# Kernel optimization log

Hardware: AMD Instinct MI355X
Metric: run time of the kernel (lower is better)

The kernel has to match this reference:

```python
import jax, jax.numpy as jnp
from jax import lax
import numpy as np

B, T, H, W = 8, 32, 128, 128
D_MODEL, D_STATE, D_CONV, EXPAND = 256, 16, 4, 2
D_INNER = EXPAND * D_MODEL
DT_RANK = 16  # ceil(d_model/16)
CHANS = [3, 32, 64, 96]
COV_SCALE = 0.01


def setup_inputs() -> dict:
    key = jax.random.key(0)
    ks = iter(jax.random.split(key, 64))
    def n(shape, s=0.02):
        return jax.random.normal(next(ks), shape, dtype=jnp.float32) * s
    inp = {
        "frames": jax.random.normal(next(ks), (B, T, 3, H, W), dtype=jnp.float32),
        "target_bboxes": jax.random.uniform(next(ks), (B, T, 4), dtype=jnp.float32),
    }
    for i in range(3):
        inp[f"conv_w{i}"] = n((CHANS[i + 1], CHANS[i], 3, 3, 3))
        inp[f"conv_b{i}"] = jnp.zeros((CHANS[i + 1],), jnp.float32)
        inp[f"bn_g{i}"] = jnp.ones((CHANS[i + 1],), jnp.float32)
        inp[f"bn_b{i}"] = jnp.zeros((CHANS[i + 1],), jnp.float32)
    inp["ep_w"] = n((D_MODEL, CHANS[-1])); inp["ep_b"] = jnp.zeros((D_MODEL,), jnp.float32)
    inp["bp1_w"] = n((64, 4), 0.1); inp["bp1_b"] = jnp.zeros((64,), jnp.float32)
    inp["bp2_w"] = n((D_MODEL, 64)); inp["bp2_b"] = jnp.zeros((D_MODEL,), jnp.float32)
    inp["in_proj_w"] = n((2 * D_INNER, D_MODEL))
    inp["conv1d_w"] = n((D_INNER, 1, D_CONV), 0.1)
    inp["conv1d_b"] = jnp.zeros((D_INNER,), jnp.float32)
    inp["x_proj_w"] = n((DT_RANK + 2 * D_STATE, D_INNER))
    inp["dt_proj_w"] = n((D_INNER, DT_RANK), 0.1)
    inp["dt_proj_b"] = jnp.full((D_INNER,), -3.0, jnp.float32)
    inp["A_log"] = jnp.log(jnp.broadcast_to(jnp.arange(1, D_STATE + 1, dtype=jnp.float32), (D_INNER, D_STATE)))
    inp["D_param"] = jnp.ones((D_INNER,), jnp.float32)
    inp["out_proj_w"] = n((D_MODEL, D_INNER))
    inp["h1_w"] = n((D_MODEL // 2, D_MODEL)); inp["h1_b"] = jnp.zeros((D_MODEL // 2,), jnp.float32)
    inp["h2_w"] = n((4, D_MODEL // 2), 0.1); inp["h2_b"] = jnp.zeros((4,), jnp.float32)
    inp["kf_F"] = jnp.eye(4, dtype=jnp.float32) + n((4, 4), 0.01)
    inp["kf_H"] = jnp.eye(4, dtype=jnp.float32) + n((4, 4), 0.01)
    inp["kf_log_q"] = n((4,), 1.0) - 2.0
    inp["kf_log_r"] = n((4,), 1.0) - 2.0
    return inp


DN3D = ("NCDHW", "OIDHW", "NCDHW")


def _forward(frames, target_bboxes, conv_w0, conv_b0, bn_g0, bn_b0,
             conv_w1, conv_b1, bn_g1, bn_b1, conv_w2, conv_b2, bn_g2, bn_b2,
             ep_w, ep_b, bp1_w, bp1_b, bp2_w, bp2_b,
             in_proj_w, conv1d_w, conv1d_b, x_proj_w, dt_proj_w, dt_proj_b,
             A_log, D_param, out_proj_w, h1_w, h1_b, h2_w, h2_b,
             kf_F, kf_H, kf_log_q, kf_log_r):
    Bn, Tn = frames.shape[0], frames.shape[1]

    # ---- bbox_proj: Linear(4,64) -> ReLU -> Linear(64,d_model) ----
    bf = jax.nn.relu(target_bboxes @ bp1_w.T + bp1_b) @ bp2_w.T + bp2_b  # (B,T,Dm)

    # ---- 3D conv encoder (BN in eval mode: running stats 0/1 -> affine only) ----
    x = jnp.transpose(frames, (0, 2, 1, 3, 4))  # (B,C,T,H,W)
    for (w, b, g, be) in ((conv_w0, conv_b0, bn_g0, bn_b0),
                          (conv_w1, conv_b1, bn_g1, bn_b1),
                          (conv_w2, conv_b2, bn_g2, bn_b2)):
        x = lax.conv_general_dilated(x, w, (1, 2, 2), ((1, 1), (1, 1), (1, 1)),
                                     dimension_numbers=DN3D) + b[None, :, None, None, None]
        x = g[None, :, None, None, None] * x + be[None, :, None, None, None]
        x = jax.nn.relu(x)
        x = lax.reduce_window(x, -jnp.inf, lax.max, (1, 1, 1, 2, 2), (1, 1, 1, 2, 2), "VALID")
    x = x.mean(axis=(3, 4))                    # AdaptiveAvgPool3d((None,1,1)) -> (B,Cenc,T)
    ff = jnp.transpose(x, (0, 2, 1)) @ ep_w.T + ep_b  # (B,T,Dm)

    u = ff + bf

    # ---- Mamba block ----
    xz = u @ in_proj_w.T                        # (B,T,2*Di)
    xm, z = jnp.split(xz, 2, axis=-1)
    xc = jnp.transpose(xm, (0, 2, 1))           # (B,Di,T)
    xc = lax.conv_general_dilated(xc, conv1d_w, (1,), ((D_CONV - 1, 0),),
                                  dimension_numbers=("NCW", "OIW", "NCW"),
                                  feature_group_count=D_INNER) + conv1d_b[None, :, None]
    xs = jax.nn.silu(jnp.transpose(xc, (0, 2, 1)))  # (B,T,Di)
    xdbl = xs @ x_proj_w.T
    dt, Bm, Cm = jnp.split(xdbl, [DT_RANK, DT_RANK + D_STATE], axis=-1)
    dt = jax.nn.softplus(dt @ dt_proj_w.T + dt_proj_b)    # (B,T,Di)
    A = -jnp.exp(A_log)                                    # (Di,Ds)
    dA = jnp.exp(dt[..., None] * A)                        # (B,T,Di,Ds)
    dBx = dt[..., None] * Bm[:, :, None, :] * xs[..., None]

    def ssm_step(h, inputs):
        dA_t, dBx_t, C_t = inputs
        h = dA_t * h + dBx_t                               # (B,Di,Ds)
        y = jnp.einsum("bds,bs->bd", h, C_t)
        return h, y

    h0 = jnp.zeros((Bn, D_INNER, D_STATE), xs.dtype)
    _, ys = lax.scan(ssm_step, h0, (jnp.transpose(dA, (1, 0, 2, 3)),
                                    jnp.transpose(dBx, (1, 0, 2, 3)),
                                    jnp.transpose(Cm, (1, 0, 2))))
    y = jnp.transpose(ys, (1, 0, 2)) + D_param * xs
    y = y * jax.nn.silu(z)
    mo = y @ out_proj_w.T                                  # (B,T,Dm)

    # ---- measurement head ----
    meas = jax.nn.sigmoid(jax.nn.relu(mo @ h1_w.T + h1_b) @ h2_w.T + h2_b)  # (B,T,4)

    # ---- Kalman filter over T (scan) ----
    Q = jnp.diag(jnp.exp(kf_log_q) + 1e-6)
    R = jnp.diag(jnp.exp(kf_log_r) + 1e-6)
    I4 = jnp.eye(4, dtype=meas.dtype)
    Hb = jnp.broadcast_to(kf_H, (Bn, 4, 4))

    def kf_step(carry, m_t):
        s, P = carry
        s_pred = jnp.einsum("ij,bjk->bik", kf_F, s)
        P_pred = jnp.einsum("ij,bjk,lk->bil", kf_F, P, kf_F) + Q
        yres = m_t - jnp.einsum("ij,bjk->bik", kf_H, s_pred)
        S = jnp.einsum("ij,bjk,lk->bil", kf_H, P_pred, kf_H) + R
        SinvH = jnp.linalg.solve(S, Hb)                    # S^{-1} H
        K = jnp.einsum("bij,bkj->bik", P_pred, SinvH)      # P H^T S^{-T}
        s_new = s_pred + K @ yres
        IKH = I4 - K @ kf_H
        P_new = IKH @ P_pred @ jnp.swapaxes(IKH, -1, -2) + (K @ R) @ jnp.swapaxes(K, -1, -2)
        return (s_new, P_new), s_new[..., 0]

    state0 = target_bboxes[:, 0, :, None]                  # (B,4,1)
    cov0 = jnp.broadcast_to(I4 * COV_SCALE, (Bn, 4, 4))
    _, preds = lax.scan(kf_step, (state0, cov0), jnp.transpose(meas, (1, 0, 2))[..., None])
    kf_pred = jnp.transpose(preds, (1, 0, 2))              # (B,T,4)
    return kf_pred, meas


def reference(frames, target_bboxes, conv_w0, conv_b0, bn_g0, bn_b0,
              conv_w1, conv_b1, bn_g1, bn_b1, conv_w2, conv_b2, bn_g2, bn_b2,
              ep_w, ep_b, bp1_w, bp1_b, bp2_w, bp2_b,
              in_proj_w, conv1d_w, conv1d_b, x_proj_w, dt_proj_w, dt_proj_b,
              A_log, D_param, out_proj_w, h1_w, h1_b, h2_w, h2_b,
              kf_F, kf_H, kf_log_q, kf_log_r):
    return _forward(frames, target_bboxes, conv_w0, conv_b0, bn_g0, bn_b0,
                    conv_w1, conv_b1, bn_g1, bn_b1, conv_w2, conv_b2, bn_g2, bn_b2,
                    ep_w, ep_b, bp1_w, bp1_b, bp2_w, bp2_b,
                    in_proj_w, conv1d_w, conv1d_b, x_proj_w, dt_proj_w, dt_proj_b,
                    A_log, D_param, out_proj_w, h1_w, h1_b, h2_w, h2_b,
                    kf_F, kf_H, kf_log_q, kf_log_r)
```

## Files before the change

### kernel.cpp

```cpp
#include <hip/hip_runtime.h>
#include <math.h>

constexpr int Bn = 8, Tn = 32;
constexpr int D_INNER = 512;

typedef __attribute__((ext_vector_type(8))) short short8;
typedef __attribute__((ext_vector_type(8))) unsigned short ushort8;
typedef __attribute__((ext_vector_type(4))) float f32x4;

__device__ inline unsigned short f2bf(float x) {
    unsigned int u = __float_as_uint(x);
    unsigned int r = (u + 0x7FFF + ((u >> 16) & 1)) >> 16;
    return (unsigned short)r;
}

__device__ __forceinline__ float kf_mm(float Av, float Bv, int i, int j, int gb) {
    float c = 0.f;
    #pragma unroll
    for (int k = 0; k < 4; ++k)
        c = fmaf(__shfl(Av, gb + i * 4 + k, 64), __shfl(Bv, gb + k * 4 + j, 64), c);
    return c;
}
__device__ __forceinline__ float kf_mmT(float Av, float Bv, int i, int j, int gb) {
    float c = 0.f;
    #pragma unroll
    for (int k = 0; k < 4; ++k)
        c = fmaf(__shfl(Av, gb + i * 4 + k, 64), __shfl(Bv, gb + j * 4 + k, 64), c);
    return c;
}

__global__ void prep_all(
    const float* __restrict__ cw0, const float* __restrict__ cw1,
    const float* __restrict__ cw2,
    const float* __restrict__ ip, const float* __restrict__ xp,
    const float* __restrict__ dt, const float* __restrict__ op,
    const float* __restrict__ h1, const float* __restrict__ h2,
    const float* __restrict__ ep, const float* __restrict__ bp2,
    const float* __restrict__ bp1,
    const float* __restrict__ kfF, const float* __restrict__ kfH,
    const float* __restrict__ lq, const float* __restrict__ lr,
    unsigned short* __restrict__ w0b, unsigned short* __restrict__ w1b,
    unsigned short* __restrict__ w2b, float* __restrict__ tW,
    float* __restrict__ kfK)
{
    int idx = blockIdx.x * blockDim.x + threadIdx.x;
    if (idx < 9216) {
        int d = idx;
        int sl = d & 7, sq = (d >> 3) & 3, co = (d >> 5) & 31;
        int r = d >> 10; int ky = r % 3, kt = r / 3;
        int q = sq ^ (co & 3) ^ ((co >> 2) & 3);
        float v = 0.f;
        if (q < 3 && sl < 3)
            v = cw0[((((size_t)co * 3 + sl) * 3 + kt) * 3 + ky) * 3 + q];
        w0b[d] = f2bf(v);
    } else if (idx < 64512) {
        int d = idx - 9216;
        int sl = d & 7, sg = (d >> 3) & 3, co = (d >> 5) & 63;
        int r = d >> 11; int k9 = r % 9, kt = r / 9;
        int ci = (sg ^ (co & 3)) * 8 + sl;
        w1b[d] = f2bf(cw1[((size_t)(co * 32 + ci) * 3 + kt) * 9 + k9]);
    } else if (idx < 230400) {
        int d = idx - 64512;
        int cip = d & 31; int rest = d >> 5;
        int co = rest % 96; rest /= 96;
        int k9 = rest % 9; int hh = rest / 9;
        int h = hh & 1, kt = hh >> 1;
        int ci = h * 32 + cip;
        w2b[d] = f2bf(cw2[((size_t)(co * 64 + ci) * 3 + kt) * 9 + k9]);
    } else if (idx < 730880) {
        int d = idx - 230400;
        const float* src; int N, K, base;
        if      (d < 262144) { src = ip;  N = 1024; K = 256; base = 0; }
        else if (d < 286720) { src = xp;  N = 48;   K = 512; base = 262144; }
        else if (d < 294912) { src = dt;  N = 512;  K = 16;  base = 286720; }
        else if (d < 425984) { src = op;  N = 256;  K = 512; base = 294912; }
        else if (d < 458752) { src = h1;  N = 128;  K = 256; base = 425984; }
        else if (d < 459264) { src = h2;  N = 4;    K = 128; base = 458752; }
        else if (d < 483840) { src = ep;  N = 256;  K = 96;  base = 459264; }
        else if (d < 500224) { src = bp2; N = 256;  K = 64;  base = 483840; }
        else                 { src = bp1; N = 64;   K = 4;   base = 500224; }
        int s = d - base;
        int o = s / K, k = s - o * K;
        tW[base + k * N + o] = src[s];
    } else {
        if (threadIdx.x >= 64) return;
        int l16 = threadIdx.x & 15;
        int i = l16 >> 2, j = l16 & 3;
        int gb = threadIdx.x & 48;
        float Fv = kfF[l16], Hv = kfH[l16];
        float R4[4];
        #pragma unroll
        for (int k = 0; k < 4; ++k) R4[k] = expf(lr[k]) + 1e-6f;
        float qi = expf(lq[i]) + 1e-6f;
        float Pv = (i == j) ? 0.01f : 0.f;
        for (int t = 0; t < Tn; ++t) {
            float FPv = kf_mm(Fv, Pv, i, j, gb);
            float Ppv = kf_mmT(FPv, Fv, i, j, gb) + ((i == j) ? qi : 0.f);
            float HPv = kf_mm(Hv, Ppv, i, j, gb);
            float Sv = kf_mmT(HPv, Hv, i, j, gb) + ((i == j) ? R4[i] : 0.f);
            float Xv = Hv;
            #pragma unroll
            for (int c = 0; c < 4; ++c) {
                float piv = __shfl(Sv, gb + c * 5, 64);
                float dinv = 1.f / piv;
                if (i == c) { Sv *= dinv; Xv *= dinv; }
                float Scj = __shfl(Sv, gb + c * 4 + j, 64);
                float Xcj = __shfl(Xv, gb + c * 4 + j, 64);
                float f = __shfl(Sv, gb + i * 4 + c, 64);
                if (i != c) { Sv = fmaf(-f, Scj, Sv); Xv = fmaf(-f, Xcj, Xv); }
            }
            float Kv = kf_mmT(Ppv, Xv, i, j, gb);
            if (threadIdx.x < 16) kfK[t * 16 + l16] = Kv;
            float IKHv = ((i == j) ? 1.f : 0.f) - kf_mm(Kv, Hv, i, j, gb);
            float T1v = kf_mm(IKHv, Ppv, i, j, gb);
            float krk = 0.f;
            #pragma unroll
            for (int k = 0; k < 4; ++k)
                krk = fmaf(__shfl(Kv, gb + i * 4 + k, 64) * R4[k],
                           __shfl(Kv, gb + j * 4 + k, 64), krk);
            Pv = kf_mmT(T1v, IKHv, i, j, gb) + krk;
        }
    }
}

constexpr int C0_STR  = 68;
constexpr int C0_BLKS = 17 * C0_STR;

__global__ __launch_bounds__(512) void conv0_kernel(
    const float* __restrict__ in, const unsigned short* __restrict__ w0b,
    const float* __restrict__ bias, const float* __restrict__ gam,
    const float* __restrict__ bet, unsigned short* __restrict__ out)
{
    int tid  = threadIdx.x;
    int lane = tid & 63;
    int wv   = __builtin_amdgcn_readfirstlane(tid >> 6);
    int q    = lane >> 4;
    int l15  = lane & 15;
    int pyp  = wv >> 1;
    int hx   = wv & 1;
    int bI = blockIdx.x;
    int bt = bI >> 4, yt = (bI >> 1) & 7, xh = bI & 1;
    int b = bt >> 5, t = bt & 31;

    __shared__ __align__(16) unsigned short S[C0_BLKS * 8];
    __shared__ __align__(16) unsigned short W[9 * 32 * 32];

    f32x4 acc[2][2];
    #pragma unroll
    for (int dy = 0; dy < 2; ++dy)
        #pragma unroll
        for (int nt = 0; nt < 2; ++nt) acc[dy][nt] = (f32x4)0.f;

    {
        const uint4* wsrc = (const uint4*)w0b;
        uint4* wdst = (uint4*)W;
        for (int e = tid; e < 1152; e += 512) wdst[e] = wsrc[e];
    }

    int oxl = hx * 16 + l15;

    int offs[3]; bool oksp[3];
    #pragma unroll
    for (int i = 0; i < 3; ++i) {
        int e = tid + 512 * i;
        int r = e / C0_STR, c = e - r * C0_STR;
        int gy = 16 * yt - 1 + r;
        int x  = 64 * xh + c - 1;
        bool act = (e < C0_BLKS);
        oksp[i] = act && gy >= 0 && gy < 128 && x >= 0 && x < 128;
        offs[i] = gy * 128 + x;
    }

    float biv[2] = {bias[l15], bias[l15 + 16]};
    float gv [2] = {gam [l15], gam [l15 + 16]};
    float bev[2] = {bet [l15], bet [l15 + 16]};

    float pf[3][3];
    auto ldG = [&](int ts) {
        bool tok = ((unsigned)ts < (unsigned)Tn);
        const float* base = in + (size_t)(b * Tn + (tok ? ts : 0)) * 49152;
        #pragma unroll
        for (int i = 0; i < 3; ++i) {
            bool ok = tok && oksp[i];
            const float* p = base + offs[i];
            pf[i][0] = ok ? p[0]     : 0.f;
            pf[i][1] = ok ? p[16384] : 0.f;
            pf[i][2] = ok ? p[32768] : 0.f;
        }
    };
    auto stS = [&]() {
        #pragma unroll
        for (int i = 0; i < 3; ++i) {
            if (i < 2 || tid < C0_BLKS - 1024) {
                unsigned w0_, w1_;
                asm("v_cvt_pk_bf16_f32 %0, %1, %2" : "=v"(w0_) : "v"(pf[i][0]), "v"(pf[i][1]));
                asm("v_cvt_pk_bf16_f32 %0, %1, %2" : "=v"(w1_) : "v"(pf[i][2]), "v"(0.f));
                uint4 pk; pk.x = w0_; pk.y = w1_; pk.z = 0u; pk.w = 0u;
                *(uint4*)(S + (size_t)(tid + 512 * i) * 8) = pk;
            }
        }
    };
    auto compute = [&](int kt) {
        #pragma unroll
        for (int ky = 0; ky < 3; ++ky) {
            short8 bfr[2];
            #pragma unroll
            for (int nt = 0; nt < 2; ++nt) {
                int co = nt * 16 + l15;
                int i16 = ((kt * 3 + ky) * 32 + co) * 4 +
                          (q ^ (co & 3) ^ ((co >> 2) & 3));
                bfr[nt] = *(const short8*)(W + (size_t)i16 * 8);
            }
            #pragma unroll
            for (int dy = 0; dy < 2; ++dy) {
                int r = 4 * pyp + 2 * dy + ky;
                short8 af = (short8)0;
                if (q < 3)
                    af = *(const short8*)(S + (size_t)(r * C0_STR + 2 * oxl + q) * 8);
                #pragma unroll
                for (int nt = 0; nt < 2; ++nt)
                    acc[dy][nt] = __builtin_amdgcn_mfma_f32_16x16x32_bf16(
                        af, bfr[nt], acc[dy][nt], 0, 0, 0);
            }
        }
    };

    ldG(t - 1);
    stS();
    ldG(t);
    __syncthreads();
    compute(0);
    __syncthreads();
    stS();
    ldG(t + 1);
    __syncthreads();
    compute(1);
    __syncthreads();
    stS();
    __syncthreads();
    compute(2);

    unsigned short* dst = out + (size_t)bt * 32768;
    #pragma unroll
    for (int nt = 0; nt < 2; ++nt) {
        int co = nt * 16 + l15;
        float bi = biv[nt], g = gv[nt], be = bev[nt];
        #pragma unroll
        for (int j = 0; j < 2; ++j) {
            float m0 = fmaxf(fmaf(g, acc[0][nt][2 * j]     + bi, be), 0.f);
            float m1 = fmaxf(fmaf(g, acc[0][nt][2 * j + 1] + bi, be), 0.f);
            float m2 = fmaxf(fmaf(g, acc[1][nt][2 * j]     + bi, be), 0.f);
            float m3 = fmaxf(fmaf(g, acc[1][nt][2 * j + 1] + bi, be), 0.f);
            float p = fmaxf(fmaxf(m0, m1), fmaxf(m2, m3));
            int pox = xh * 16 + hx * 8 + q * 2 + j;
            int poy = yt * 4 + pyp;
            dst[(poy * 32 + pox) * 32 + co] = f2bf(p);
        }
    }
}

__global__ __launch_bounds__(512) void conv1_kernel(
    const unsigned short* __restrict__ in, const unsigned short* __restrict__ w1b,
    const float* __restrict__ bias, const float* __restrict__ gam,
    const float* __restrict__ bet, unsigned short* __restrict__ out)
{
    int tid  = threadIdx.x;
    int lane = tid & 63;
    int wv   = tid >> 6;
    int q    = lane >> 4;
    int l15  = lane & 15;
    int oyp  = wv >> 1;
    int nh   = wv & 1;
    int bt = blockIdx.x >> 1, half = blockIdx.x & 1;
    int b = bt >> 5, t = bt & 31;

    __shared__ __align__(16) unsigned short S[17 * 34 * 32];
    __shared__ __align__(16) unsigned short W[9 * 64 * 32];

    f32x4 acc[2][2];
    #pragma unroll
    for (int mt = 0; mt < 2; ++mt)
        #pragma unroll
        for (int nt = 0; nt < 2; ++nt) acc[mt][nt] = (f32x4)0.f;

    for (int kt = 0; kt < 3; ++kt) {
        int ts = t + kt - 1;
        if (ts < 0 || ts >= Tn) continue;
        __syncthreads();
        const unsigned short* src = in + (size_t)(b * Tn + ts) * 32768;
        for (int e = tid; e < 17 * 34 * 4; e += 512) {
            int sb = e & 3;
            int pos = e >> 2;
            int ys = pos / 34, xs = pos - ys * 34;
            int g = sb ^ ((xs >> 1) & 3);
            int y = 16 * half + ys - 1, x = xs - 1;
            ushort8 v = (ushort8)0;
            if (y >= 0 && x >= 0 && x < 32)
                v = *(const ushort8*)(src + ((y * 32 + x) * 32 + g * 8));
            *(ushort8*)(S + (size_t)e * 8) = v;
        }
        {
            const uint4* wsrc = (const uint4*)(w1b + kt * 18432);
            uint4* wdst = (uint4*)W;
            for (int e = tid; e < 2304; e += 512) wdst[e] = wsrc[e];
        }
        __syncthreads();

        for (int k9 = 0; k9 < 9; ++k9) {
            int ky = k9 / 3, kx = k9 - ky * 3;
            short8 bf[2];
            #pragma unroll
            for (int nt = 0; nt < 2; ++nt) {
                int co = nh * 32 + nt * 16 + l15;
                int blk = (k9 * 64 + co) * 4 + (q ^ (co & 3));
                bf[nt] = *(const short8*)(W + blk * 8);
            }
            short8 af[2];
            #pragma unroll
            for (int mt = 0; mt < 2; ++mt) {
                int oyl = 2 * oyp + mt;
                int ys = 2 * oyl + ky;
                int xs = 2 * l15 + kx;
                int blk = (ys * 34 + xs) * 4 + (q ^ ((xs >> 1) & 3));
                af[mt] = *(const short8*)(S + blk * 8);
            }
            #pragma unroll
            for (int mt = 0; mt < 2; ++mt)
                #pragma unroll
                for (int nt = 0; nt < 2; ++nt)
                    acc[mt][nt] = __builtin_amdgcn_mfma_f32_16x16x32_bf16(
                        af[mt], bf[nt], acc[mt][nt], 0, 0, 0);
        }
    }

    unsigned short* dst = out + (size_t)bt * 4096;
    #pragma unroll
    for (int nt = 0; nt < 2; ++nt) {
        int co = nh * 32 + nt * 16 + l15;
        float bi = bias[co], g = gam[co], be = bet[co];
        #pragma unroll
        for (int j = 0; j < 2; ++j) {
            float m0 = fmaxf(fmaf(g, acc[0][nt][2 * j]     + bi, be), 0.f);
            float m1 = fmaxf(fmaf(g, acc[0][nt][2 * j + 1] + bi, be), 0.f);
            float m2 = fmaxf(fmaf(g, acc[1][nt][2 * j]     + bi, be), 0.f);
            float m3 = fmaxf(fmaf(g, acc[1][nt][2 * j + 1] + bi, be), 0.f);
            float p = fmaxf(fmaxf(m0, m1), fmaxf(m2, m3));
            int px = 2 * q + j, py = half * 4 + oyp;
            dst[(py * 8 + px) * 64 + co] = f2bf(p);
        }
    }
}

__global__ __launch_bounds__(384) void conv2_kernel(
    const unsigned short* __restrict__ in, const unsigned short* __restrict__ w2b,
    const float* __restrict__ bias, const float* __restrict__ gam,
    const float* __restrict__ bet, float* __restrict__ out)
{
    int tid  = threadIdx.x;
    int lane = tid & 63;
    int wv   = tid >> 6;
    int q    = lane >> 4;
    int l15  = lane & 15;
    int bt = blockIdx.x;
    int b = bt >> 5, t = bt & 31;

    __shared__ __align__(16) unsigned short W[864 * 5 * 8];
    __shared__ __align__(16) unsigned short S[81 * 5 * 8];

    f32x4 acc = (f32x4)0.f;

    for (int kt = 0; kt < 3; ++kt) {
        int ts = t + kt - 1;
        if (ts < 0 || ts >= Tn) continue;
        for (int h = 0; h < 2; ++h) {
            __syncthreads();
            const unsigned short* wsrc = w2b + (size_t)((kt * 2 + h) * 9) * 96 * 32;
            for (int e = tid; e < 3456; e += 384) {
                int r = e >> 2, qq = e & 3;
                uint4 v = *(const uint4*)(wsrc + r * 32 + qq * 8);
                *(uint4*)(W + (r * 5 + qq) * 8) = v;
            }
            const unsigned short* src = in + (size_t)(b * Tn + ts) * 4096 + h * 32;
            for (int e = tid; e < 81 * 4; e += 384) {
                int cb = e & 3, p = e >> 2;
                int ys = p / 9, xs = p - ys * 9;
                int y = ys - 1, x = xs - 1;
                ushort8 v = (ushort8)0;
                if (y >= 0 && x >= 0 && y < 8 && x < 8)
                    v = *(const ushort8*)(src + ((y * 8 + x) * 64 + cb * 8));
                *(ushort8*)(S + (size_t)(p * 5 + cb) * 8) = v;
            }
            __syncthreads();

            int oy = l15 >> 2, ox = l15 & 3;
            #pragma unroll
            for (int k9 = 0; k9 < 9; ++k9) {
                int ky = k9 / 3, kx = k9 - ky * 3;
                short8 bf = *(const short8*)(W + (size_t)((k9 * 96 + wv * 16 + l15) * 5 + q) * 8);
                int p = (2 * oy + ky) * 9 + (2 * ox + kx);
                short8 af = *(const short8*)(S + (size_t)(p * 5 + q) * 8);
                acc = __builtin_amdgcn_mfma_f32_16x16x32_bf16(af, bf, acc, 0, 0, 0);
            }
        }
    }

    int co = wv * 16 + l15;
    float bi = bias[co], g = gam[co], be = bet[co];
    float v0 = fmaxf(fmaf(g, acc[0] + bi, be), 0.f);
    float v1 = fmaxf(fmaf(g, acc[1] + bi, be), 0.f);
    float v2 = fmaxf(fmaf(g, acc[2] + bi, be), 0.f);
    float v3 = fmaxf(fmaf(g, acc[3] + bi, be), 0.f);
    float p0 = fmaxf(v0, v1);
    float p1 = fmaxf(v2, v3);
    float r0 = fmaxf(p0, __shfl_xor(p0, 16));
    float r1 = fmaxf(p1, __shfl_xor(p1, 16));
    if ((q & 1) == 0) {
        int py = q >> 1;
        float* o = out + (size_t)(bt * 96 + co) * 4 + py * 2;
        o[0] = r0;
        o[1] = r1;
    }
}

__global__ __launch_bounds__(256) void fuse_u_inproj(
    const float* __restrict__ buf2, const float* __restrict__ epT,
    const float* __restrict__ ep_b, const float* __restrict__ bb,
    const float* __restrict__ bp1T, const float* __restrict__ bp1_b,
    const float* __restrict__ bp2T, const float* __restrict__ bp2_b,
    const float* __restrict__ ipwT, float* __restrict__ xzb)
{
    int bt = blockIdx.x;
    int m  = threadIdx.x;
    __shared__ float hs[64];
    __shared__ float gap[96];
    __shared__ float u_lds[256];
    if (m < 64) {
        float a = bp1_b[m];
        #pragma unroll
        for (int k = 0; k < 4; ++k) a = fmaf(bp1T[k * 64 + m], bb[bt * 4 + k], a);
        hs[m] = fmaxf(a, 0.f);
    } else if (m < 160) {
        int c = m - 64;
        const float* p = buf2 + ((size_t)bt * 96 + c) * 4;
        gap[c] = 0.25f * (p[0] + p[1] + p[2] + p[3]);
    }
    __syncthreads();
    float ff = ep_b[m];
    for (int c = 0; c < 96; ++c) ff = fmaf(gap[c], epT[c * 256 + m], ff);
    float bfv = bp2_b[m];
    for (int j = 0; j < 64; ++j) bfv = fmaf(hs[j], bp2T[j * 256 + m], bfv);
    u_lds[m] = ff + bfv;
    __syncthreads();

    const float4* wbase = (const float4*)ipwT + m;
    float4 acc = {0.f, 0.f, 0.f, 0.f};
    for (int k = 0; k < 256; ++k) {
        float uk = u_lds[k];
        float4 w4 = wbase[(size_t)k * 256];
        acc.x = fmaf(uk, w4.x, acc.x);
        acc.y = fmaf(uk, w4.y, acc.y);
        acc.z = fmaf(uk, w4.z, acc.z);
        acc.w = fmaf(uk, w4.w, acc.w);
    }
    *(float4*)(xzb + (size_t)bt * 1024 + 4 * m) = acc;
}

__global__ __launch_bounds__(512) void convxd_kernel(
    const float* __restrict__ xzb, const float* __restrict__ c1w,
    const float* __restrict__ c1b, const float* __restrict__ xpw,
    const float* __restrict__ dtwT, const float* __restrict__ dt_b,
    float* __restrict__ xsb, float* __restrict__ xdb, float* __restrict__ dtbf)
{
    int bt = blockIdx.x;
    int b = bt >> 5, t = bt & 31;
    int tid = threadIdx.x;
    __shared__ float xs_lds[512];
    __shared__ float xd_lds[48];

    {
        float acc = c1b[tid];
        #pragma unroll
        for (int k = 0; k < 4; ++k) {
            int ts = t - 3 + k;
            if (ts >= 0)
                acc = fmaf(c1w[tid * 4 + k], xzb[(size_t)(b * Tn + ts) * 1024 + tid], acc);
        }
        float v = acc / (1.f + expf(-acc));
        xs_lds[tid] = v;
        xsb[(size_t)bt * 512 + tid] = v;
    }
    __syncthreads();

    {
        int wv = tid >> 6, ln = tid & 63;
        #pragma unroll
        for (int u = 0; u < 6; ++u) {
            int o = wv * 6 + u;
            const float* wrow = xpw + (size_t)o * 512;
            float acc = 0.f;
            #pragma unroll
            for (int e = 0; e < 8; ++e)
                acc = fmaf(wrow[ln + 64 * e], xs_lds[ln + 64 * e], acc);
            acc += __shfl_xor(acc, 32); acc += __shfl_xor(acc, 16);
            acc += __shfl_xor(acc, 8);  acc += __shfl_xor(acc, 4);
            acc += __shfl_xor(acc, 2);  acc += __shfl_xor(acc, 1);
            if (ln == 0) {
                xd_lds[o] = acc;
                xdb[(size_t)bt * 48 + o] = acc;
            }
        }
    }
    __syncthreads();

    {
        float a = dt_b[tid];
        #pragma unroll
        for (int k = 0; k < 16; ++k) a = fmaf(xd_lds[k], dtwT[k * 512 + tid], a);
        a = (a > 20.f) ? a : log1pf(expf(a));
        dtbf[(size_t)bt * 512 + tid] = a;
    }
}

__global__ __launch_bounds__(256) void ssm_kernel(
    const float* __restrict__ xdbl, const float* __restrict__ dtb,
    const float* __restrict__ xs, const float* __restrict__ xz,
    const float* __restrict__ A_log, const float* __restrict__ Dp,
    float* __restrict__ y)
{
    int tid = threadIdx.x;
    int lane = tid & 63;
    int s = lane & 15, dsub = lane >> 4;
    int gid = blockIdx.x * 4 + (tid >> 6);
    int b = gid >> 7;
    int d = ((gid & 127) << 2) + dsub;

    float A = -expf(A_log[d * 16 + s]);
    float Dv = Dp[d];
    float h = 0.f;
    for (int t = 0; t < Tn; ++t) {
        int bt = b * Tn + t;
        float dtv = dtb[(size_t)bt * 512 + d];
        float xv  = xs [(size_t)bt * 512 + d];
        float Bs  = xdbl[(size_t)bt * 48 + 16 + s];
        float Cs  = xdbl[(size_t)bt * 48 + 32 + s];
        float dA = expf(dtv * A);
        h = fmaf(dA, h, dtv * Bs * xv);
        float c = h * Cs;
        c += __shfl_xor(c, 8, 16);
        c += __shfl_xor(c, 4, 16);
        c += __shfl_xor(c, 2, 16);
        c += __shfl_xor(c, 1, 16);
        if (s == 0) {
            float zv = xz[(size_t)bt * 1024 + 512 + d];
            float sig = 1.f / (1.f + expf(-zv));
            y[(size_t)bt * 512 + d] = (c + Dv * xv) * (zv * sig);
        }
    }
}

__global__ __launch_bounds__(256) void out_head_kernel(
    const float* __restrict__ yb, const float* __restrict__ opwT,
    const float* __restrict__ h1wT, const float* __restrict__ h1_b,
    const float* __restrict__ h2w, const float* __restrict__ h2_b,
    float* __restrict__ meas_out)
{
    int bt = blockIdx.x;
    int m  = threadIdx.x;
    __shared__ float y_lds[512];
    __shared__ float mo_lds[256];
    __shared__ float hid_lds[128];

    y_lds[m]       = yb[(size_t)bt * 512 + m];
    y_lds[m + 256] = yb[(size_t)bt * 512 + m + 256];
    __syncthreads();

    {
        float a = 0.f;
        for (int k = 0; k < 512; ++k) a = fmaf(y_lds[k], opwT[k * 256 + m], a);
        mo_lds[m] = a;
    }
    __syncthreads();

    if (m < 128) {
        float a = h1_b[m];
        for (int k = 0; k < 256; ++k) a = fmaf(mo_lds[k], h1wT[k * 128 + m], a);
        hid_lds[m] = fmaxf(a, 0.f);
    }
    __syncthreads();

    if (m < 64) {
        int o2 = m >> 4, l15 = m & 15;
        float acc = 0.f;
        #pragma unroll
        for (int e = 0; e < 8; ++e)
            acc = fmaf(h2w[o2 * 128 + l15 + 16 * e], hid_lds[l15 + 16 * e], acc);
        acc += __shfl_xor(acc, 8, 16);
        acc += __shfl_xor(acc, 4, 16);
        acc += __shfl_xor(acc, 2, 16);
        acc += __shfl_xor(acc, 1, 16);
        if (l15 == 0) {
            float a = acc + h2_b[o2];
            meas_out[bt * 4 + o2] = 1.f / (1.f + expf(-a));
        }
    }
}

__global__ __launch_bounds__(128) void kf_kernel(
    const float* __restrict__ meas, const float* __restrict__ bb,
    const float* __restrict__ Fin, const float* __restrict__ Hmin,
    const float* __restrict__ kfK, float* __restrict__ pred)
{
    int tid = threadIdx.x;
    int b   = tid >> 4;
    int l16 = tid & 15;
    int i = l16 >> 2, j = l16 & 3;
    int gb = tid & 48;

    float Fv = Fin[l16], Hv = Hmin[l16];
    float sv = bb[b * 128 + j];

    for (int t = 0; t < Tn; ++t) {
        float mv = meas[(b * Tn + t) * 4 + j];
        float Kv = kfK[t * 16 + l16];
        float tr = Fv * sv;
        tr += __shfl_xor(tr, 1); tr += __shfl_xor(tr, 2);
        float spv = tr;
        float spj = __shfl(spv, gb + j * 4, 64);
        float hsp = Hv * spj;
        hsp += __shfl_xor(hsp, 1); hsp += __shfl_xor(hsp, 2);
        float yrv = mv - __shfl(hsp, gb + j * 4, 64);
        float t3 = Kv * yrv;
        t3 += __shfl_xor(t3, 1); t3 += __shfl_xor(t3, 2);
        float snv = spv + t3;
        if (j == 0) pred[(b * Tn + t) * 4 + i] = snv;
        sv = __shfl(snv, gb + j * 4, 64);
    }
}

extern "C" void kernel_launch(void* const* d_in, const int* in_sizes, int n_in,
                              void* d_out, int out_size, void* d_ws, size_t ws_size,
                              hipStream_t stream)
{
    const float* frames = (const float*)d_in[0];
    const float* bb     = (const float*)d_in[1];
    const float* cw0 = (const float*)d_in[2],  *cb0 = (const float*)d_in[3];
    const float* g0  = (const float*)d_in[4],  *be0 = (const float*)d_in[5];
    const float* cw1 = (const float*)d_in[6],  *cb1 = (const float*)d_in[7];
    const float* g1  = (const float*)d_in[8],  *be1 = (const float*)d_in[9];
    const float* cw2 = (const float*)d_in[10], *cb2 = (const float*)d_in[11];
    const float* g2  = (const float*)d_in[12], *be2 = (const float*)d_in[13];
    const float* ep_w  = (const float*)d_in[14], *ep_b  = (const float*)d_in[15];
    const float* bp1_w = (const float*)d_in[16], *bp1_b = (const float*)d_in[17];
    const float* bp2_w = (const float*)d_in[18], *bp2_b = (const float*)d_in[19];
    const float* in_proj_w = (const float*)d_in[20];
    const float* c1w = (const float*)d_in[21], *c1b = (const float*)d_in[22];
    const float* x_proj_w = (const float*)d_in[23];
    const float* dt_w = (const float*)d_in[24], *dt_b = (const float*)d_in[25];
    const float* A_log = (const float*)d_in[26], *Dp = (const float*)d_in[27];
    const float* out_proj_w = (const float*)d_in[28];
    const float* h1_w = (const float*)d_in[29], *h1_b = (const float*)d_in[30];
    const float* h2_w = (const float*)d_in[31], *h2_b = (const float*)d_in[32];
    const float* kfF = (const float*)d_in[33], *kfH = (const float*)d_in[34];
    const float* kfq = (const float*)d_in[35], *kfr = (const float*)d_in[36];

    float* ws   = (float*)d_ws;
    float* buf2 = ws;
    float* xzb  = buf2 + 98304;
    float* xsb  = xzb  + 262144;
    float* xdb  = xsb  + 131072;
    float* dtbf = xdb  + 12288;
    float* yb   = dtbf + 131072;
    float* tW   = yb   + 131072;
    float* kfK  = tW + 500480;
    unsigned short* buf0b = (unsigned short*)(kfK + 512);
    unsigned short* buf1b = buf0b + 8388608;
    unsigned short* w2b   = buf1b + 131072;
    unsigned short* w1b   = w2b + 165888;
    unsigned short* w0b   = w1b + 55296;

    float* ipwT = tW;
    float* dtwT = tW + 286720;
    float* opwT = tW + 294912;
    float* h1wT = tW + 425984;
    float* epwT = tW + 459264;
    float* bp2T = tW + 483840;
    float* bp1T = tW + 500224;

    float* kf_out   = (float*)d_out;
    float* meas_out = kf_out + Bn * Tn * 4;

    prep_all<<<dim3(2856), 256, 0, stream>>>(cw0, cw1, cw2,
                                             in_proj_w, x_proj_w, dt_w, out_proj_w,
                                             h1_w, h2_w, ep_w, bp2_w, bp1_w,
                                             kfF, kfH, kfq, kfr,
                                             w0b, w1b, w2b, tW, kfK);

    conv0_kernel<<<dim3(4096), 512, 0, stream>>>(frames, w0b, cb0, g0, be0, buf0b);
    conv1_kernel<<<dim3(512), 512, 0, stream>>>(buf0b, w1b, cb1, g1, be1, buf1b);
    conv2_kernel<<<dim3(256), 384, 0, stream>>>(buf1b, w2b, cb2, g2, be2, buf2);

    fuse_u_inproj<<<dim3(256), 256, 0, stream>>>(buf2, epwT, ep_b, bb, bp1T, bp1_b,
                                                 bp2T, bp2_b, ipwT, xzb);
    convxd_kernel<<<dim3(256), 512, 0, stream>>>(xzb, c1w, c1b, x_proj_w,
                                                 dtwT, dt_b, xsb, xdb, dtbf);
    ssm_kernel<<<dim3(256), 256, 0, stream>>>(xdb, dtbf, xsb, xzb, A_log, Dp, yb);
    out_head_kernel<<<dim3(256), 256, 0, stream>>>(yb, opwT, h1wT, h1_b,
                                                   h2_w, h2_b, meas_out);
    kf_kernel<<<dim3(1), 128, 0, stream>>>(meas_out, bb, kfF, kfH, kfK, kf_out);
}
```

Baseline: 326.3 us.

## Widen in-projection and output-head blocks and prefetch SSM inputs ahead

The in-projection kernel now uses 1024 threads, so each thread computes one output column instead of a float4 of four. The output-head kernel doubles its threads and splits the K reductions of out_proj and h1 into partial sums that are combined through shared memory. The SSM scan loop software-prefetches its per-timestep inputs three steps ahead to hide global load latency along the serial recurrence. These changes add parallelism and latency hiding in small per-token kernels, at the cost of larger blocks, extra syncs and higher register use.

```diff
diff --git a/kernel.cpp b/kernel.cpp
--- a/kernel.cpp
+++ b/kernel.cpp
@@ -422,47 +422,44 @@
     }
 }
 
-__global__ __launch_bounds__(256) void fuse_u_inproj(
+__global__ __launch_bounds__(1024) void fuse_u_inproj(
     const float* __restrict__ buf2, const float* __restrict__ epT,
     const float* __restrict__ ep_b, const float* __restrict__ bb,
     const float* __restrict__ bp1T, const float* __restrict__ bp1_b,
     const float* __restrict__ bp2T, const float* __restrict__ bp2_b,
     const float* __restrict__ ipwT, float* __restrict__ xzb)
 {
-    int bt = blockIdx.x;
-    int m  = threadIdx.x;
+    int bt  = blockIdx.x;
+    int tid = threadIdx.x;
     __shared__ float hs[64];
     __shared__ float gap[96];
     __shared__ float u_lds[256];
-    if (m < 64) {
-        float a = bp1_b[m];
-        #pragma unroll
-        for (int k = 0; k < 4; ++k) a = fmaf(bp1T[k * 64 + m], bb[bt * 4 + k], a);
-        hs[m] = fmaxf(a, 0.f);
-    } else if (m < 160) {
-        int c = m - 64;
+    if (tid < 64) {
+        float a = bp1_b[tid];
+        #pragma unroll
+        for (int k = 0; k < 4; ++k) a = fmaf(bp1T[k * 64 + tid], bb[bt * 4 + k], a);
+        hs[tid] = fmaxf(a, 0.f);
+    } else if (tid < 160) {
+        int c = tid - 64;
         const float* p = buf2 + ((size_t)bt * 96 + c) * 4;
         gap[c] = 0.25f * (p[0] + p[1] + p[2] + p[3]);
     }
     __syncthreads();
-    float ff = ep_b[m];
-    for (int c = 0; c < 96; ++c) ff = fmaf(gap[c], epT[c * 256 + m], ff);
-    float bfv = bp2_b[m];
-    for (int j = 0; j < 64; ++j) bfv = fmaf(hs[j], bp2T[j * 256 + m], bfv);
-    u_lds[m] = ff + bfv;
-    __syncthreads();
-
-    const float4* wbase = (const float4*)ipwT + m;
-    float4 acc = {0.f, 0.f, 0.f, 0.f};
-    for (int k = 0; k < 256; ++k) {
-        float uk = u_lds[k];
-        float4 w4 = wbase[(size_t)k * 256];
-        acc.x = fmaf(uk, w4.x, acc.x);
-        acc.y = fmaf(uk, w4.y, acc.y);
-        acc.z = fmaf(uk, w4.z, acc.z);
-        acc.w = fmaf(uk, w4.w, acc.w);
-    }
-    *(float4*)(xzb + (size_t)bt * 1024 + 4 * m) = acc;
+    if (tid < 256) {
+        float ff = ep_b[tid];
+        for (int c = 0; c < 96; ++c) ff = fmaf(gap[c], epT[c * 256 + tid], ff);
+        float bfv = bp2_b[tid];
+        for (int j = 0; j < 64; ++j) bfv = fmaf(hs[j], bp2T[j * 256 + tid], bfv);
+        u_lds[tid] = ff + bfv;
+    }
+    __syncthreads();
+
+    const float* w = ipwT + tid;
+    float acc = 0.f;
+    #pragma unroll 8
+    for (int k = 0; k < 256; ++k)
+        acc = fmaf(u_lds[k], w[(size_t)k * 1024], acc);
+    xzb[(size_t)bt * 1024 + tid] = acc;
 }
 
 __global__ __launch_bounds__(512) void convxd_kernel(
@@ -537,12 +534,29 @@
     float A = -expf(A_log[d * 16 + s]);
     float Dv = Dp[d];
     float h = 0.f;
+
+    auto ld = [&](int t, float& dtv, float& xv, float& Bs, float& Cs) {
+        int bt = b * Tn + t;
+        dtv = dtb[(size_t)bt * 512 + d];
+        xv  = xs [(size_t)bt * 512 + d];
+        Bs  = xdbl[(size_t)bt * 48 + 16 + s];
+        Cs  = xdbl[(size_t)bt * 48 + 32 + s];
+    };
+
+    float c_dt, c_x, c_B, c_C;
+    float n1_dt, n1_x, n1_B, n1_C;
+    float n2_dt, n2_x, n2_B, n2_C;
+    ld(0, c_dt, c_x, c_B, c_C);
+    ld(1, n1_dt, n1_x, n1_B, n1_C);
+    ld(2, n2_dt, n2_x, n2_B, n2_C);
+
     for (int t = 0; t < Tn; ++t) {
         int bt = b * Tn + t;
-        float dtv = dtb[(size_t)bt * 512 + d];
-        float xv  = xs [(size_t)bt * 512 + d];
-        float Bs  = xdbl[(size_t)bt * 48 + 16 + s];
-        float Cs  = xdbl[(size_t)bt * 48 + 32 + s];
+        float dtv = c_dt, xv = c_x, Bs = c_B, Cs = c_C;
+        c_dt = n1_dt; c_x = n1_x; c_B = n1_B; c_C = n1_C;
+        n1_dt = n2_dt; n1_x = n2_x; n1_B = n2_B; n1_C = n2_C;
+        if (t + 3 < Tn) ld(t + 3, n2_dt, n2_x, n2_B, n2_C);
+
         float dA = expf(dtv * A);
         h = fmaf(dA, h, dtv * Bs * xv);
         float c = h * Cs;
@@ -558,38 +572,55 @@
     }
 }
 
-__global__ __launch_bounds__(256) void out_head_kernel(
+__global__ __launch_bounds__(512) void out_head_kernel(
     const float* __restrict__ yb, const float* __restrict__ opwT,
     const float* __restrict__ h1wT, const float* __restrict__ h1_b,
     const float* __restrict__ h2w, const float* __restrict__ h2_b,
     float* __restrict__ meas_out)
 {
-    int bt = blockIdx.x;
-    int m  = threadIdx.x;
+    int bt  = blockIdx.x;
+    int tid = threadIdx.x;
     __shared__ float y_lds[512];
+    __shared__ float part[512];
     __shared__ float mo_lds[256];
+    __shared__ float hpart[512];
     __shared__ float hid_lds[128];
 
-    y_lds[m]       = yb[(size_t)bt * 512 + m];
-    y_lds[m + 256] = yb[(size_t)bt * 512 + m + 256];
+    y_lds[tid] = yb[(size_t)bt * 512 + tid];
     __syncthreads();
 
     {
+        int m = tid & 255, hh = tid >> 8;
         float a = 0.f;
-        for (int k = 0; k < 512; ++k) a = fmaf(y_lds[k], opwT[k * 256 + m], a);
-        mo_lds[m] = a;
-    }
-    __syncthreads();
-
-    if (m < 128) {
-        float a = h1_b[m];
-        for (int k = 0; k < 256; ++k) a = fmaf(mo_lds[k], h1wT[k * 128 + m], a);
-        hid_lds[m] = fmaxf(a, 0.f);
-    }
-    __syncthreads();
-
-    if (m < 64) {
-        int o2 = m >> 4, l15 = m & 15;
+        const float* wcol = opwT + m;
+        int k0 = hh * 256;
+        for (int k = k0; k < k0 + 256; ++k)
+            a = fmaf(y_lds[k], wcol[(size_t)k * 256], a);
+        part[hh * 256 + m] = a;
+    }
+    __syncthreads();
+    if (tid < 256) mo_lds[tid] = part[tid] + part[256 + tid];
+    __syncthreads();
+
+    {
+        int m = tid & 127, qq = tid >> 7;
+        float a = 0.f;
+        const float* wcol = h1wT + m;
+        int k0 = qq * 64;
+        for (int k = k0; k < k0 + 64; ++k)
+            a = fmaf(mo_lds[k], wcol[(size_t)k * 128], a);
+        hpart[qq * 128 + m] = a;
+    }
+    __syncthreads();
+    if (tid < 128) {
+        float a = h1_b[tid] + (hpart[tid] + hpart[128 + tid]) +
+                              (hpart[256 + tid] + hpart[384 + tid]);
+        hid_lds[tid] = fmaxf(a, 0.f);
+    }
+    __syncthreads();
+
+    if (tid < 64) {
+        int o2 = tid >> 4, l15 = tid & 15;
         float acc = 0.f;
         #pragma unroll
         for (int e = 0; e < 8; ++e)
@@ -699,12 +730,12 @@
     conv1_kernel<<<dim3(512), 512, 0, stream>>>(buf0b, w1b, cb1, g1, be1, buf1b);
     conv2_kernel<<<dim3(256), 384, 0, stream>>>(buf1b, w2b, cb2, g2, be2, buf2);
 
-    fuse_u_inproj<<<dim3(256), 256, 0, stream>>>(buf2, epwT, ep_b, bb, bp1T, bp1_b,
-                                                 bp2T, bp2_b, ipwT, xzb);
+    fuse_u_inproj<<<dim3(256), 1024, 0, stream>>>(buf2, epwT, ep_b, bb, bp1T, bp1_b,
+                                                  bp2T, bp2_b, ipwT, xzb);
     convxd_kernel<<<dim3(256), 512, 0, stream>>>(xzb, c1w, c1b, x_proj_w,
                                                  dtwT, dt_b, xsb, xdb, dtbf);
     ssm_kernel<<<dim3(256), 256, 0, stream>>>(xdb, dtbf, xsb, xzb, A_log, Dp, yb);
-    out_head_kernel<<<dim3(256), 256, 0, stream>>>(yb, opwT, h1wT, h1_b,
+    out_head_kernel<<<dim3(256), 512, 0, stream>>>(yb, opwT, h1wT, h1_b,
                                                    h2_w, h2_b, meas_out);
     kf_kernel<<<dim3(1), 128, 0, stream>>>(meas_out, bb, kfF, kfH, kfK, kf_out);
 }
```

New measurement: 378.1 us. +15.9%, slower.

## Split fused u/in_proj kernel into u kernel plus tiled in_proj GEMM

Applied to the files above, without the earlier changes.

Splits the fused kernel, which streamed the full 1 MB transposed in_proj weight once per token across 256 blocks, into two kernels. The first computes the u vectors into a global buffer. The second is a 16x16-tiled GEMM over all 256 tokens that loads the original in_proj_w rows into LDS, so weight traffic is shared across 16 tokens per tile. This cuts global weight reads but adds a kernel launch and a round trip of u through global memory. The transposed ipwT copy is no longer used by this path.

```diff
diff --git a/kernel.cpp b/kernel.cpp
--- a/kernel.cpp
+++ b/kernel.cpp
@@ -422,47 +422,75 @@
     }
 }
 
-__global__ __launch_bounds__(256) void fuse_u_inproj(
+__global__ __launch_bounds__(128) void u_kernel(
     const float* __restrict__ buf2, const float* __restrict__ epT,
     const float* __restrict__ ep_b, const float* __restrict__ bb,
     const float* __restrict__ bp1T, const float* __restrict__ bp1_b,
     const float* __restrict__ bp2T, const float* __restrict__ bp2_b,
-    const float* __restrict__ ipwT, float* __restrict__ xzb)
-{
-    int bt = blockIdx.x;
-    int m  = threadIdx.x;
+    float* __restrict__ u_glob)
+{
+    int bt   = blockIdx.x >> 1;
+    int half = blockIdx.x & 1;
+    int tid  = threadIdx.x;
     __shared__ float hs[64];
     __shared__ float gap[96];
-    __shared__ float u_lds[256];
-    if (m < 64) {
-        float a = bp1_b[m];
-        #pragma unroll
-        for (int k = 0; k < 4; ++k) a = fmaf(bp1T[k * 64 + m], bb[bt * 4 + k], a);
-        hs[m] = fmaxf(a, 0.f);
-    } else if (m < 160) {
-        int c = m - 64;
-        const float* p = buf2 + ((size_t)bt * 96 + c) * 4;
-        gap[c] = 0.25f * (p[0] + p[1] + p[2] + p[3]);
-    }
-    __syncthreads();
+    if (tid < 96) {
+        const float* p = buf2 + ((size_t)bt * 96 + tid) * 4;
+        gap[tid] = 0.25f * (p[0] + p[1] + p[2] + p[3]);
+    }
+    if (tid < 64) {
+        float a = bp1_b[tid];
+        #pragma unroll
+        for (int k = 0; k < 4; ++k) a = fmaf(bp1T[k * 64 + tid], bb[bt * 4 + k], a);
+        hs[tid] = fmaxf(a, 0.f);
+    }
+    __syncthreads();
+    int m = half * 128 + tid;
     float ff = ep_b[m];
+    #pragma unroll 4
     for (int c = 0; c < 96; ++c) ff = fmaf(gap[c], epT[c * 256 + m], ff);
     float bfv = bp2_b[m];
+    #pragma unroll 4
     for (int j = 0; j < 64; ++j) bfv = fmaf(hs[j], bp2T[j * 256 + m], bfv);
-    u_lds[m] = ff + bfv;
-    __syncthreads();
-
-    const float4* wbase = (const float4*)ipwT + m;
-    float4 acc = {0.f, 0.f, 0.f, 0.f};
-    for (int k = 0; k < 256; ++k) {
-        float uk = u_lds[k];
-        float4 w4 = wbase[(size_t)k * 256];
-        acc.x = fmaf(uk, w4.x, acc.x);
-        acc.y = fmaf(uk, w4.y, acc.y);
-        acc.z = fmaf(uk, w4.z, acc.z);
-        acc.w = fmaf(uk, w4.w, acc.w);
-    }
-    *(float4*)(xzb + (size_t)bt * 1024 + 4 * m) = acc;
+    u_glob[(size_t)bt * 256 + m] = ff + bfv;
+}
+
+__global__ __launch_bounds__(256) void inproj_gemm(
+    const float* __restrict__ u_glob, const float* __restrict__ ip,
+    float* __restrict__ xzb)
+{
+    int bid = blockIdx.x;
+    int nt = bid & 63, mt = bid >> 6;
+    int tid = threadIdx.x;
+
+    __shared__ float Ut[16 * 257];
+    __shared__ float Wt[16 * 257];
+
+    {
+        const float4* us = (const float4*)(u_glob + (size_t)mt * 16 * 256);
+        const float4* ws = (const float4*)(ip + (size_t)nt * 16 * 256);
+        #pragma unroll
+        for (int i = 0; i < 4; ++i) {
+            int idx = tid + 256 * i;
+            int row = idx >> 6, col4 = idx & 63;
+            float4 uv = us[idx];
+            float4 wv = ws[idx];
+            float* ud = Ut + row * 257 + col4 * 4;
+            float* wd = Wt + row * 257 + col4 * 4;
+            ud[0] = uv.x; ud[1] = uv.y; ud[2] = uv.z; ud[3] = uv.w;
+            wd[0] = wv.x; wd[1] = wv.y; wd[2] = wv.z; wd[3] = wv.w;
+        }
+    }
+    __syncthreads();
+
+    int out_l = tid & 15, tok_l = tid >> 4;
+    const float* ur = Ut + tok_l * 257;
+    const float* wr = Wt + out_l * 257;
+    float acc = 0.f;
+    #pragma unroll 8
+    for (int k = 0; k < 256; ++k)
+        acc = fmaf(ur[k], wr[k], acc);
+    xzb[(size_t)(mt * 16 + tok_l) * 1024 + nt * 16 + out_l] = acc;
 }
 
 __global__ __launch_bounds__(512) void convxd_kernel(
@@ -672,7 +700,8 @@
     float* yb   = dtbf + 131072;
     float* tW   = yb   + 131072;
     float* kfK  = tW + 500480;
-    unsigned short* buf0b = (unsigned short*)(kfK + 512);
+    float* u_glob = kfK + 512;
+    unsigned short* buf0b = (unsigned short*)(u_glob + 65536);
     unsigned short* buf1b = buf0b + 8388608;
     unsigned short* w2b   = buf1b + 131072;
     unsigned short* w1b   = w2b + 165888;
@@ -699,8 +728,9 @@
     conv1_kernel<<<dim3(512), 512, 0, stream>>>(buf0b, w1b, cb1, g1, be1, buf1b);
     conv2_kernel<<<dim3(256), 384, 0, stream>>>(buf1b, w2b, cb2, g2, be2, buf2);
 
-    fuse_u_inproj<<<dim3(256), 256, 0, stream>>>(buf2, epwT, ep_b, bb, bp1T, bp1_b,
-                                                 bp2T, bp2_b, ipwT, xzb);
+    u_kernel<<<dim3(512), 128, 0, stream>>>(buf2, epwT, ep_b, bb, bp1T, bp1_b,
+                                            bp2T, bp2_b, u_glob);
+    inproj_gemm<<<dim3(1024), 256, 0, stream>>>(u_glob, in_proj_w, xzb);
     convxd_kernel<<<dim3(256), 512, 0, stream>>>(xzb, c1w, c1b, x_proj_w,
                                                  dtwT, dt_b, xsb, xdb, dtbf);
     ssm_kernel<<<dim3(256), 256, 0, stream>>>(xdb, dtbf, xsb, xzb, A_log, Dp, yb);
```

New measurement: 332.9 us. 2.0% more time.
